# Optimization experiments

Measured on AMD Instinct MI355X. Metric: run time of the kernel, lower is better.

Reference implementation:

```python
import jax, jax.numpy as jnp
import numpy as np

WH, WW = 14, 14
NUM_HEADS = 12
HEAD_DIM = 64
HIDDEN = NUM_HEADS * HEAD_DIM
SEQ = WH * WW + 1  # 197, includes cls token
NUM_REL = (2 * WH - 1) * (2 * WW - 1) + 3  # 732


def _relative_position_index(wh, ww):
    # Static numpy computation, identical to BeitRelativePositionBias buffer
    coords = np.stack(np.meshgrid(np.arange(wh), np.arange(ww), indexing='ij'))  # [2, wh, ww]
    flat = coords.reshape(2, -1)  # [2, wh*ww]
    rel = flat[:, :, None] - flat[:, None, :]  # [2, N, N]
    rel = rel.transpose(1, 2, 0).astype(np.int64)  # [N, N, 2]
    rel[..., 0] += wh - 1
    rel[..., 1] += ww - 1
    rel[..., 0] *= 2 * ww - 1
    nrd = (2 * wh - 1) * (2 * ww - 1) + 3
    idx = np.zeros((wh * ww + 1, wh * ww + 1), dtype=np.int64)
    idx[1:, 1:] = rel.sum(-1)
    idx[0, :] = nrd - 3
    idx[:, 0] = nrd - 2
    idx[0, 0] = nrd - 1
    return idx

_REL_IDX = jnp.asarray(_relative_position_index(WH, WW))  # [SEQ, SEQ]


def setup_inputs() -> dict:
    key = jax.random.key(0)
    ks = jax.random.split(key, 7)
    B = 64
    s = 1.0 / np.sqrt(HIDDEN)
    return {
        'hidden_states': jax.random.normal(ks[0], (B, SEQ, HIDDEN), jnp.float32),
        'Wq': jax.random.normal(ks[1], (HIDDEN, HIDDEN), jnp.float32) * s,
        'bq': jax.random.normal(ks[2], (HIDDEN,), jnp.float32) * 0.02,
        'Wk': jax.random.normal(ks[3], (HIDDEN, HIDDEN), jnp.float32) * s,
        'Wv': jax.random.normal(ks[4], (HIDDEN, HIDDEN), jnp.float32) * s,
        'bv': jax.random.normal(ks[5], (HIDDEN,), jnp.float32) * 0.02,
        'bias_table': jax.random.normal(ks[6], (NUM_REL, NUM_HEADS), jnp.float32) * 0.02,
    }


def reference(hidden_states, Wq, bq, Wk, Wv, bv, bias_table):
    B, S, D = hidden_states.shape
    H, Dh = NUM_HEADS, HEAD_DIM

    def heads(x):  # [B,S,D] -> [B,H,S,Dh]
        return x.reshape(B, S, H, Dh).transpose(0, 2, 1, 3)

    q = heads(hidden_states @ Wq + bq)
    k = heads(hidden_states @ Wk)           # key projection has no bias
    v = heads(hidden_states @ Wv + bv)

    scores = jnp.einsum('bhqd,bhkd->bhqk', q, k) / jnp.sqrt(jnp.float32(Dh))
    # relative position bias: gather [SEQ,SEQ,H] -> [H,SEQ,SEQ]
    rel_bias = bias_table[_REL_IDX].transpose(2, 0, 1)
    scores = scores + rel_bias[None]

    probs = jax.nn.softmax(scores, axis=-1)  # dropout prob = 0 (eval)
    ctx = jnp.einsum('bhqk,bhkd->bhqd', probs, v)
    ctx = ctx.transpose(0, 2, 1, 3).reshape(B, S, D)
    return ctx
```

## Files before the change

kernel.cpp:

```cpp
#include <hip/hip_runtime.h>
#include <hip/hip_bf16.h>
#include <stdint.h>

typedef unsigned short u16;
typedef __attribute__((ext_vector_type(4))) float f32x4;
typedef __attribute__((ext_vector_type(8))) short s16x8;
typedef __attribute__((ext_vector_type(4))) unsigned short u16x4;
typedef __attribute__((ext_vector_type(4))) float fvec4;

#define NH 12
#define DH 64
#define HID 768
#define SEQ 197
#define VP 224
#define NREL 732
#define BATCH 64
#define MROWS (BATCH*SEQ)
#define NCAT (3*HID)
#define BK 64
#define MT 99
#define NT 18
#define NWG (MT*NT)
#define QKSTRIDE (SEQ*DH)

#define PB_X 4728
#define PB_W (PB_X + 432)
#define PB_B (PB_W + 9)
#define PB_E (PB_B + 2028)

static __device__ __forceinline__ u16 f2bf(float f) {
  union { float f; uint32_t u; } v; v.f = f;
  uint32_t u = v.u;
  return (u16)((u + 0x7FFFu + ((u >> 16) & 1u)) >> 16);
}
static __device__ __forceinline__ float bf2f(u16 v) {
  union { uint32_t u; float f; } x; x.u = ((uint32_t)v) << 16; return x.f;
}

__global__ __launch_bounds__(256) void prep_all(const float* __restrict__ x,
                                                const float* __restrict__ Wq, const float* __restrict__ Wk,
                                                const float* __restrict__ Wv, const float* __restrict__ bq,
                                                const float* __restrict__ bv, const float* __restrict__ btab,
                                                u16* __restrict__ xb, u16* __restrict__ Wt,
                                                float* __restrict__ bc, u16* __restrict__ Bxt) {
  __shared__ float t[64][65];
  const int bi = blockIdx.x;
  const int tid = threadIdx.x;
  if (bi < PB_X) {
    int i = bi * 256 + tid;
    fvec4 a = ((const fvec4*)x)[2 * i];
    fvec4 b = ((const fvec4*)x)[2 * i + 1];
    s16x8 r;
    r[0] = (short)f2bf(a[0]); r[1] = (short)f2bf(a[1]); r[2] = (short)f2bf(a[2]); r[3] = (short)f2bf(a[3]);
    r[4] = (short)f2bf(b[0]); r[5] = (short)f2bf(b[1]); r[6] = (short)f2bf(b[2]); r[7] = (short)f2bf(b[3]);
    ((s16x8*)xb)[i] = r;
  } else if (bi < PB_W) {
    int f = bi - PB_X;
    int n0 = (f % 36) * 64, k0 = (f / 36) * 64;
    int m = n0 / HID;
    const float* W = (m == 0) ? Wq : ((m == 1) ? Wk : Wv);
    int nn0 = n0 - m * HID;
    for (int i = tid; i < 64 * 64; i += 256) {
      int r = i >> 6, c = i & 63;
      t[r][c] = W[(size_t)(k0 + r) * HID + nn0 + c];
    }
    __syncthreads();
    for (int i = tid; i < 64 * 64; i += 256) {
      int r = i >> 6, c = i & 63;
      Wt[(size_t)(n0 + r) * HID + k0 + c] = f2bf(t[c][r]);
    }
  } else if (bi < PB_B) {
    int i = (bi - PB_W) * 256 + tid;
    if (i < NCAT) {
      int m = i / HID, r = i - m * HID;
      bc[i] = (m == 0) ? bq[r] : ((m == 2) ? bv[r] : 0.f);
    }
  } else {
    int i = (bi - PB_B) * 256 + tid;
    int h = i / (208 * 208);
    int r = i - h * 208 * 208;
    int k = r / 208, q = r - k * 208;
    float v;
    if (k >= SEQ) v = -1e30f;
    else if (q >= SEQ) v = 0.f;
    else {
      int idx;
      if (q == 0) idx = (k == 0) ? 731 : 729;
      else if (k == 0) idx = 730;
      else {
        int iq = (q - 1) / 14, jq = (q - 1) % 14;
        int ik = (k - 1) / 14, jk = (k - 1) % 14;
        idx = (iq - ik + 13) * 27 + (jq - jk + 13);
      }
      v = btab[(size_t)idx * NH + h];
    }
    Bxt[i] = f2bf(v);
  }
}

static __device__ __forceinline__ void stage128(const u16* __restrict__ gbase, int grow0, int growmax,
                                                u16* lds, int w, int l) {
#pragma unroll
  for (int i = 0; i < 4; ++i) {
    int ch = w * 4 + i;
    int r = ch * 8 + (l >> 3);
    int grow = grow0 + r; if (grow > growmax) grow = growmax;
    int c = (l & 7) ^ (l >> 3);
    const u16* g = gbase + (size_t)grow * HID + c * 8;
    __builtin_amdgcn_global_load_lds((const __attribute__((address_space(1))) void*)g,
                                     (__attribute__((address_space(3))) void*)(lds + ch * 512),
                                     16, 0, 0);
  }
}

static __device__ __forceinline__ void compute128(const u16* As, const u16* Bs, int wr, int wc,
                                                  int li, int lg, f32x4 acc[4][4]) {
#pragma unroll
  for (int kk = 0; kk < 2; ++kk) {
    s16x8 af[4], bf[4];
#pragma unroll
    for (int mi = 0; mi < 4; ++mi) {
      int r = wr * 64 + mi * 16 + li;
      int c = (kk * 4 + lg) ^ (r & 7);
      af[mi] = *(const s16x8*)((const char*)As + r * 128 + c * 16);
    }
#pragma unroll
    for (int ni = 0; ni < 4; ++ni) {
      int r = wc * 64 + ni * 16 + li;
      int c = (kk * 4 + lg) ^ (r & 7);
      bf[ni] = *(const s16x8*)((const char*)Bs + r * 128 + c * 16);
    }
#pragma unroll
    for (int mi = 0; mi < 4; ++mi)
#pragma unroll
      for (int ni = 0; ni < 4; ++ni)
        acc[mi][ni] = __builtin_amdgcn_mfma_f32_16x16x32_bf16(af[mi], bf[ni], acc[mi][ni], 0, 0, 0);
  }
}

__global__ __launch_bounds__(256, 2) void qkv_gemm(const u16* __restrict__ Xb, const u16* __restrict__ Wt,
                                                   const float* __restrict__ bc, u16* __restrict__ Qw,
                                                   u16* __restrict__ Kw, u16* __restrict__ Vt) {
  __shared__ u16 LDSU[32768];
  u16* As0 = LDSU;
  u16* Bs0 = LDSU + 8192;
  u16* As1 = LDSU + 16384;
  u16* Bs1 = LDSU + 24576;
  const int tid = threadIdx.x;
  const int w = tid >> 6, l = tid & 63;
  const int wr = w >> 1, wc = w & 1;
  const int lg = l >> 4, li = l & 15;

  const int lin = blockIdx.x;
  const int xcd = lin & 7;
  const int pos = lin >> 3;
  const int work = (xcd < 6 ? xcd * 223 : 6 * 223 + (xcd - 6) * 222) + pos;
  const int mt = work / NT, nt = work - mt * NT;
  const int arow0 = mt * 128, brow0 = nt * 128;

  f32x4 acc[4][4] = {};

  stage128(Xb, arow0, MROWS - 1, As0, w, l);
  stage128(Wt, brow0, NCAT - 1, Bs0, w, l);
  __syncthreads();

  for (int kt2 = 0; kt2 < 6; ++kt2) {
    const int kt = kt2 * 2;
    stage128(Xb + (kt + 1) * BK, arow0, MROWS - 1, As1, w, l);
    stage128(Wt + (kt + 1) * BK, brow0, NCAT - 1, Bs1, w, l);
    compute128(As0, Bs0, wr, wc, li, lg, acc);
    __syncthreads();
    if (kt2 < 5) {
      stage128(Xb + (kt + 2) * BK, arow0, MROWS - 1, As0, w, l);
      stage128(Wt + (kt + 2) * BK, brow0, NCAT - 1, Bs0, w, l);
    }
    compute128(As1, Bs1, wr, wc, li, lg, acc);
    __syncthreads();
  }

  const int mblk = nt / 6;
  float bcv[4];
#pragma unroll
  for (int ni = 0; ni < 4; ++ni) bcv[ni] = bc[brow0 + wc * 64 + ni * 16 + li];

  if (mblk < 2) {
    u16* __restrict__ dst = (mblk == 0) ? Qw : Kw;
    const float scale = (mblk == 0) ? 0.125f : 1.0f;
    int hv[4], dv[4];
#pragma unroll
    for (int ni = 0; ni < 4; ++ni) {
      int cloc = brow0 - mblk * HID + wc * 64 + ni * 16 + li;
      hv[ni] = cloc >> 6; dv[ni] = cloc & 63;
    }
#pragma unroll
    for (int mi = 0; mi < 4; ++mi) {
#pragma unroll
      for (int j = 0; j < 4; ++j) {
        int row = arow0 + wr * 64 + mi * 16 + lg * 4 + j;
        if (row < MROWS) {
          int b = row / SEQ, s = row - b * SEQ;
#pragma unroll
          for (int ni = 0; ni < 4; ++ni)
            dst[((size_t)(b * NH + hv[ni]) * SEQ + s) * DH + dv[ni]] = f2bf((acc[mi][ni][j] + bcv[ni]) * scale);
        }
      }
    }
  } else {
#pragma unroll
    for (int mi = 0; mi < 4; ++mi) {
#pragma unroll
      for (int ni = 0; ni < 4; ++ni) {
        u16x4 pk;
#pragma unroll
        for (int j = 0; j < 4; ++j) pk[j] = f2bf(acc[mi][ni][j] + bcv[ni]);
        *(u16x4*)&LDSU[w * 4352 + (ni * 16 + li) * 68 + mi * 16 + lg * 4] = pk;
      }
    }
    __syncthreads();
    const int cw0 = brow0 - 2 * HID;
#pragma unroll 4
    for (int p = 0; p < 64; ++p) {
      int i = p * 256 + tid;
      int r = i & 127, c = i >> 7;
      int wq = ((r >> 6) << 1) | (c >> 6);
      u16 v = LDSU[wq * 4352 + (c & 63) * 68 + (r & 63)];
      int row = arow0 + r;
      if (row < MROWS) {
        int b = row / SEQ, s = row - b * SEQ;
        int cl = cw0 + c;
        int h = cl >> 6, d = cl & 63;
        Vt[((size_t)(b * NH + h) * DH + d) * VP + s] = v;
      }
    }
  }
}

__global__ __launch_bounds__(128, 2) void attn(const u16* __restrict__ Qw, const u16* __restrict__ Kw,
                                               const u16* __restrict__ Vt, const u16* __restrict__ Bxt,
                                               float* __restrict__ out) {
  __shared__ u16 Klds[208 * 64];
  __shared__ u16 P[2][16 * 232];
  const int tid = threadIdx.x;
  const int w = tid >> 6, l = tid & 63;
  const int lg = l >> 4, li = l & 15;
  const int lin = blockIdx.x;
  const int bh = (lin & 7) * 96 + (lin >> 3);
  const int b = bh / NH, h = bh - b * NH;

  const u16* Qb = Qw + (size_t)bh * QKSTRIDE;
  const u16* Kb = Kw + (size_t)bh * QKSTRIDE;
  const u16* Vb = Vt + (size_t)bh * DH * VP;

#pragma unroll
  for (int i = 0; i < 13; ++i) {
    int ch = (w * 13 + i) * 64 + l;
    int r = ch >> 3, c = ch & 7;
    int sc = c ^ (r & 7);
    __builtin_amdgcn_global_load_lds((const __attribute__((address_space(1))) void*)
                                         (Kb + (size_t)r * DH + sc * 8),
                                     (__attribute__((address_space(3))) void*)(Klds + (size_t)ch * 8),
                                     16, 0, 0);
  }
  for (int t = l; t < 16 * 24; t += 64) {
    int rr = t / 24, cc = t - rr * 24;
    P[w][rr * 232 + 208 + cc] = 0;
  }
  __syncthreads();

  for (int it = 0; it < 7; ++it) {
    const int qf = w + 2 * it;
    if (qf >= 13) break;

    const u16* Bhp = Bxt + (size_t)h * 208 * 208 + qf * 16 + lg * 4;

    s16x8 a0 = *(const s16x8*)(Qb + (size_t)(qf * 16 + li) * DH + lg * 8);
    s16x8 a1 = *(const s16x8*)(Qb + (size_t)(qf * 16 + li) * DH + 32 + lg * 8);

    u16x4 bb[13];
#pragma unroll
    for (int kf = 0; kf < 13; ++kf)
      bb[kf] = *(const u16x4*)(Bhp + (size_t)(kf * 16 + li) * 208);

    f32x4 S[13];
#pragma unroll
    for (int kf = 0; kf < 13; ++kf) {
      int r = kf * 16 + li;
      s16x8 k0 = *(const s16x8*)((const char*)Klds + r * 128 + ((lg) ^ (r & 7)) * 16);
      s16x8 k1 = *(const s16x8*)((const char*)Klds + r * 128 + ((4 + lg) ^ (r & 7)) * 16);
      f32x4 c = {};
      c = __builtin_amdgcn_mfma_f32_16x16x32_bf16(a0, k0, c, 0, 0, 0);
      c = __builtin_amdgcn_mfma_f32_16x16x32_bf16(a1, k1, c, 0, 0, 0);
#pragma unroll
      for (int j = 0; j < 4; ++j)
        S[kf][j] = c[j] + bf2f(bb[kf][j]);
    }

    float rinv[4];
#pragma unroll
    for (int j = 0; j < 4; ++j) {
      float m = S[0][j];
#pragma unroll
      for (int kf = 1; kf < 13; ++kf) m = fmaxf(m, S[kf][j]);
      m = fmaxf(m, __shfl_xor(m, 1));
      m = fmaxf(m, __shfl_xor(m, 2));
      m = fmaxf(m, __shfl_xor(m, 4));
      m = fmaxf(m, __shfl_xor(m, 8));
      float sum = 0.f;
#pragma unroll
      for (int kf = 0; kf < 13; ++kf) {
        float p = __expf(S[kf][j] - m);
        S[kf][j] = p;
        sum += p;
      }
      sum += __shfl_xor(sum, 1);
      sum += __shfl_xor(sum, 2);
      sum += __shfl_xor(sum, 4);
      sum += __shfl_xor(sum, 8);
      rinv[j] = 1.0f / sum;
    }

#pragma unroll
    for (int kf = 0; kf < 13; ++kf)
#pragma unroll
      for (int j = 0; j < 4; ++j)
        P[w][(lg * 4 + j) * 232 + kf * 16 + li] = f2bf(S[kf][j]);

    s16x8 vb[4];
#pragma unroll
    for (int p = 0; p < 4; ++p)
      vb[p] = *(const s16x8*)(Vb + (size_t)((p / 7) * 16 + li) * VP + (p % 7) * 32 + lg * 8);
    f32x4 o[4];
#pragma unroll
    for (int nf = 0; nf < 4; ++nf) {
      f32x4 c = {};
#pragma unroll
      for (int t = 0; t < 7; ++t) {
        const int u = nf * 7 + t, slot = u & 3;
        s16x8 pa = *(const s16x8*)(&P[w][li * 232 + t * 32 + lg * 8]);
        c = __builtin_amdgcn_mfma_f32_16x16x32_bf16(pa, vb[slot], c, 0, 0, 0);
        if (u + 4 < 28) {
          const int u2 = u + 4;
          vb[slot] = *(const s16x8*)(Vb + (size_t)((u2 / 7) * 16 + li) * VP + (u2 % 7) * 32 + lg * 8);
        }
      }
      o[nf] = c;
    }
#pragma unroll
    for (int nf = 0; nf < 4; ++nf) {
#pragma unroll
      for (int j = 0; j < 4; ++j) {
        int q = qf * 16 + lg * 4 + j;
        if (q < SEQ)
          out[((size_t)(b * SEQ + q)) * HID + h * DH + nf * 16 + li] = o[nf][j] * rinv[j];
      }
    }
  }
}

extern "C" void kernel_launch(void* const* d_in, const int* in_sizes, int n_in,
                              void* d_out, int out_size, void* d_ws, size_t ws_size,
                              hipStream_t stream) {
  const float* hidden = (const float*)d_in[0];
  const float* Wq = (const float*)d_in[1];
  const float* bq = (const float*)d_in[2];
  const float* Wk = (const float*)d_in[3];
  const float* Wv = (const float*)d_in[4];
  const float* bv = (const float*)d_in[5];
  const float* btab = (const float*)d_in[6];
  float* out = (float*)d_out;

  char* ws = (char*)d_ws;
  u16* Xb  = (u16*)(ws);
  u16* Wt  = (u16*)(ws + 19365888);
  float* bc = (float*)(ws + 22904832);
  u16* Bxt = (u16*)(ws + 22914048);
  u16* Qw  = (u16*)(ws + 23952512);
  u16* Kw  = (u16*)(ws + 43322496);
  u16* Vt  = (u16*)(ws + 62692480);

  prep_all<<<dim3(PB_E), dim3(256), 0, stream>>>(hidden, Wq, Wk, Wv, bq, bv, btab, Xb, Wt, bc, Bxt);
  qkv_gemm<<<dim3(NWG), dim3(256), 0, stream>>>(Xb, Wt, bc, Qw, Kw, Vt);
  attn<<<dim3(768), dim3(128), 0, stream>>>(Qw, Kw, Vt, Bxt, out);
}
```

Baseline: 119.0 us.

## Load QKV weight fragments directly from global into registers, shrink LDS

The QKV GEMM no longer stages the weight (B) tiles through LDS. Each wave loads its B fragments straight from global memory into registers, double-buffered across k-steps. LDS then holds only the A tiles, and the occupancy hint rises from 2 to 3 blocks per CU. This cuts LDS traffic and capacity use, but adds register pressure and strided, less coalesced global loads whose latency may be exposed. Weight rows are re-read by both wr waves.

```diff
diff --git a/kernel.cpp b/kernel.cpp
--- a/kernel.cpp
+++ b/kernel.cpp
@@ -98,8 +98,9 @@
   }
 }
 
-static __device__ __forceinline__ void stage128(const u16* __restrict__ gbase, int grow0, int growmax,
-                                                u16* lds, int w, int l) {
+
+static __device__ __forceinline__ void stageA(const u16* __restrict__ gbase, int grow0, int growmax,
+                                              u16* lds, int w, int l) {
 #pragma unroll
   for (int i = 0; i < 4; ++i) {
     int ch = w * 4 + i;
@@ -113,11 +114,22 @@
   }
 }
 
-static __device__ __forceinline__ void compute128(const u16* As, const u16* Bs, int wr, int wc,
+static __device__ __forceinline__ void loadB(const u16* __restrict__ b0, const u16* __restrict__ b1,
+                                             const u16* __restrict__ b2, const u16* __restrict__ b3,
+                                             int k0, int lg, s16x8 bf[8]) {
+  const u16* rows[4] = {b0, b1, b2, b3};
+#pragma unroll
+  for (int ni = 0; ni < 4; ++ni)
+#pragma unroll
+    for (int kk = 0; kk < 2; ++kk)
+      bf[ni * 2 + kk] = *(const s16x8*)(rows[ni] + k0 + kk * 32 + lg * 8);
+}
+
+static __device__ __forceinline__ void compute_bd(const u16* As, const s16x8 bf[8], int wr,
                                                   int li, int lg, f32x4 acc[4][4]) {
 #pragma unroll
   for (int kk = 0; kk < 2; ++kk) {
-    s16x8 af[4], bf[4];
+    s16x8 af[4];
 #pragma unroll
     for (int mi = 0; mi < 4; ++mi) {
       int r = wr * 64 + mi * 16 + li;
@@ -125,27 +137,19 @@
       af[mi] = *(const s16x8*)((const char*)As + r * 128 + c * 16);
     }
 #pragma unroll
-    for (int ni = 0; ni < 4; ++ni) {
-      int r = wc * 64 + ni * 16 + li;
-      int c = (kk * 4 + lg) ^ (r & 7);
-      bf[ni] = *(const s16x8*)((const char*)Bs + r * 128 + c * 16);
-    }
-#pragma unroll
     for (int mi = 0; mi < 4; ++mi)
 #pragma unroll
       for (int ni = 0; ni < 4; ++ni)
-        acc[mi][ni] = __builtin_amdgcn_mfma_f32_16x16x32_bf16(af[mi], bf[ni], acc[mi][ni], 0, 0, 0);
-  }
-}
-
-__global__ __launch_bounds__(256, 2) void qkv_gemm(const u16* __restrict__ Xb, const u16* __restrict__ Wt,
+        acc[mi][ni] = __builtin_amdgcn_mfma_f32_16x16x32_bf16(af[mi], bf[ni * 2 + kk], acc[mi][ni], 0, 0, 0);
+  }
+}
+
+__global__ __launch_bounds__(256, 3) void qkv_gemm(const u16* __restrict__ Xb, const u16* __restrict__ Wt,
                                                    const float* __restrict__ bc, u16* __restrict__ Qw,
                                                    u16* __restrict__ Kw, u16* __restrict__ Vt) {
-  __shared__ u16 LDSU[32768];
+  __shared__ u16 LDSU[18432];
   u16* As0 = LDSU;
-  u16* Bs0 = LDSU + 8192;
-  u16* As1 = LDSU + 16384;
-  u16* Bs1 = LDSU + 24576;
+  u16* As1 = LDSU + 8192;
   const int tid = threadIdx.x;
   const int w = tid >> 6, l = tid & 63;
   const int wr = w >> 1, wc = w & 1;
@@ -158,23 +162,29 @@
   const int mt = work / NT, nt = work - mt * NT;
   const int arow0 = mt * 128, brow0 = nt * 128;
 
+  const u16* Br0 = Wt + (size_t)(brow0 + wc * 64 + 0 * 16 + li) * HID;
+  const u16* Br1 = Wt + (size_t)(brow0 + wc * 64 + 1 * 16 + li) * HID;
+  const u16* Br2 = Wt + (size_t)(brow0 + wc * 64 + 2 * 16 + li) * HID;
+  const u16* Br3 = Wt + (size_t)(brow0 + wc * 64 + 3 * 16 + li) * HID;
+
   f32x4 acc[4][4] = {};
-
-  stage128(Xb, arow0, MROWS - 1, As0, w, l);
-  stage128(Wt, brow0, NCAT - 1, Bs0, w, l);
+  s16x8 bfA[8], bfB[8];
+
+  stageA(Xb, arow0, MROWS - 1, As0, w, l);
+  loadB(Br0, Br1, Br2, Br3, 0, lg, bfA);
   __syncthreads();
 
   for (int kt2 = 0; kt2 < 6; ++kt2) {
     const int kt = kt2 * 2;
-    stage128(Xb + (kt + 1) * BK, arow0, MROWS - 1, As1, w, l);
-    stage128(Wt + (kt + 1) * BK, brow0, NCAT - 1, Bs1, w, l);
-    compute128(As0, Bs0, wr, wc, li, lg, acc);
+    stageA(Xb + (kt + 1) * BK, arow0, MROWS - 1, As1, w, l);
+    loadB(Br0, Br1, Br2, Br3, (kt + 1) * BK, lg, bfB);
+    compute_bd(As0, bfA, wr, li, lg, acc);
     __syncthreads();
     if (kt2 < 5) {
-      stage128(Xb + (kt + 2) * BK, arow0, MROWS - 1, As0, w, l);
-      stage128(Wt + (kt + 2) * BK, brow0, NCAT - 1, Bs0, w, l);
-    }
-    compute128(As1, Bs1, wr, wc, li, lg, acc);
+      stageA(Xb + (kt + 2) * BK, arow0, MROWS - 1, As0, w, l);
+      loadB(Br0, Br1, Br2, Br3, (kt + 2) * BK, lg, bfA);
+    }
+    compute_bd(As1, bfB, wr, li, lg, acc);
     __syncthreads();
   }
 
```

After: 161.8 us. +36.0%, slower.
